# Performance work log

Hardware: AMD Instinct MI355X
Metric: run time of the kernel (lower is better)

The kernel has to match this reference:

```python
import jax, jax.numpy as jnp
import numpy as np

D_MODEL = 1024
H = 16
D_K = D_MODEL // H
D_FF = 4096
EPS = 1e-6
NEG = -1.0e9


def setup_inputs() -> dict:
    key = jax.random.key(0)
    ks = jax.random.split(key, 8)
    B, S = 4, 2048
    x = jax.random.normal(ks[0], (B, S, D_MODEL), dtype=jnp.float32)
    src_mask = jnp.ones((B, 1, S, S), dtype=jnp.int32)
    s = 0.02
    wq = jax.random.normal(ks[1], (D_MODEL, D_MODEL), jnp.float32) * s
    wk = jax.random.normal(ks[2], (D_MODEL, D_MODEL), jnp.float32) * s
    wv = jax.random.normal(ks[3], (D_MODEL, D_MODEL), jnp.float32) * s
    wo = jax.random.normal(ks[4], (D_MODEL, D_MODEL), jnp.float32) * s
    w1 = jax.random.normal(ks[5], (D_MODEL, D_FF), jnp.float32) * s
    b1 = jnp.zeros((D_FF,), jnp.float32)
    w2 = jax.random.normal(ks[6], (D_FF, D_MODEL), jnp.float32) * s
    b2 = jnp.zeros((D_MODEL,), jnp.float32)
    # LayerNorm params are scalars in the original (torch.ones(1)/zeros(1))
    a1 = jnp.ones((1,), jnp.float32); bt1 = jnp.zeros((1,), jnp.float32)
    a2 = jnp.ones((1,), jnp.float32); bt2 = jnp.zeros((1,), jnp.float32)
    return {"x": x, "src_mask": src_mask, "wq": wq, "wk": wk, "wv": wv,
            "wo": wo, "w1": w1, "b1": b1, "w2": w2, "b2": b2,
            "a1": a1, "bt1": bt1, "a2": a2, "bt2": bt2}


def _layernorm(x, alpha, beta):
    # Original: (x - mean) / (std + eps), std with Bessel correction (torch default)
    mean = jnp.mean(x, axis=-1, keepdims=True)
    std = jnp.std(x, axis=-1, keepdims=True, ddof=1)
    return alpha * (x - mean) / (std + EPS) + beta


def _mha(x, mask, wq, wk, wv, wo):
    B, S, _ = x.shape
    q = (x @ wq).reshape(B, S, H, D_K).transpose(0, 2, 1, 3)  # [B,H,S,Dk]
    k = (x @ wk).reshape(B, S, H, D_K).transpose(0, 2, 1, 3)
    v = (x @ wv).reshape(B, S, H, D_K).transpose(0, 2, 1, 3)
    scores = jnp.einsum('bhqd,bhkd->bhqk', q, k) / jnp.sqrt(jnp.float32(D_K))
    scores = jnp.where(mask == 0, NEG, scores)
    attn = jax.nn.softmax(scores, axis=-1)
    out = jnp.einsum('bhqk,bhkd->bhqd', attn, v)  # [B,H,S,Dk]
    out = out.transpose(0, 2, 1, 3).reshape(B, S, D_MODEL)
    return out @ wo


def reference(x, src_mask, wq, wk, wv, wo, w1, b1, w2, b2, a1, bt1, a2, bt2):
    # Sublayer 1: self-attention with post-norm residual (dropout = eval/identity)
    attn_out = _mha(x, src_mask, wq, wk, wv, wo)
    x = _layernorm(x + attn_out, a1, bt1)
    # Sublayer 2: FFN with post-norm residual
    ffn_out = jax.nn.relu(x @ w1 + b1) @ w2 + b2
    x = _layernorm(x + ffn_out, a2, bt2)
    return x
```

## Files before the change

kernel.cpp:

```cpp
#include <hip/hip_runtime.h>
#include <stdint.h>

typedef __bf16 bf16x8 __attribute__((ext_vector_type(8)));
typedef float f32x4 __attribute__((ext_vector_type(4)));
typedef float f32x16 __attribute__((ext_vector_type(16)));
typedef unsigned short u16;
typedef u16 u16x8 __attribute__((ext_vector_type(8)));
typedef u16 u16x4 __attribute__((ext_vector_type(4)));
typedef uint32_t u32;

#define DEV __device__ __forceinline__
#define MFMA(a, b, c) __builtin_amdgcn_mfma_f32_16x16x32_bf16(a, b, c, 0, 0, 0)
#define MFMA32(a, b, c) __builtin_amdgcn_mfma_f32_32x32x16_bf16(a, b, c, 0, 0, 0)

static constexpr int B_ = 4, S_ = 2048, M_ = 8192, D_ = 1024, H_ = 16, DFF_ = 4096;

DEV u16 f2bf(float f) {
    union { float f; u32 u; } c; c.f = f;
    u32 u = c.u;
    return (u16)((u + 0x7fffu + ((u >> 16) & 1u)) >> 16);
}

DEV float bf2f(u16 v) {
    union { u32 u; float f; } c; c.u = (u32)v << 16;
    return c.f;
}

DEV u32 cvt_pk_bf16(float lo, float hi) {
    u32 r;
    asm("v_cvt_pk_bf16_f32 %0, %1, %2" : "=v"(r) : "v"(lo), "v"(hi));
    return r;
}

DEV float v_exp2(float x) {
    float r;
    asm("v_exp_f32 %0, %1" : "=v"(r) : "v"(x));
    return r;
}

DEV void gload16(void* lds, const void* g) {
    __builtin_amdgcn_global_load_lds(
        (const __attribute__((address_space(1))) unsigned int*)g,
        (__attribute__((address_space(3))) unsigned int*)lds, 16, 0, 0);
}


__global__ __launch_bounds__(256) void k_pack_amask(const int* __restrict__ m,
                                                    u32* __restrict__ bits,
                                                    u32* __restrict__ am) {
    const int lane = threadIdx.x & 63, wv = threadIdx.x >> 6;
    const int row = blockIdx.x * 4 + wv;
    const int4* s = (const int4*)(m + ((size_t)row * 64 + lane) * 32);
    u32 r = 0;
#pragma unroll
    for (int j = 0; j < 8; j++) {
        int4 v = s[j];
        r |= (u32)(v.x != 0) << (j * 4) | (u32)(v.y != 0) << (j * 4 + 1) |
             (u32)(v.z != 0) << (j * 4 + 2) | (u32)(v.w != 0) << (j * 4 + 3);
    }
    bits[(size_t)row * 64 + lane] = r;
    unsigned long long b = __ballot(r == 0xffffffffu);
    if (lane == 0) {
        u32 a = 0;
#pragma unroll
        for (int t = 0; t < 32; t++)
            a |= (u32)(((b >> (2 * t)) & 3ull) == 3ull) << t;
        am[row] = a;
    }
}

__global__ __launch_bounds__(256) void k_cast_bf16(const float* __restrict__ s,
                                                   u16* __restrict__ d, int n4) {
    int i = blockIdx.x * 256 + threadIdx.x;
    if (i >= n4) return;
    f32x4 v = ((const f32x4*)s)[i];
    u16x4 o;
    o[0] = f2bf(v[0]); o[1] = f2bf(v[1]); o[2] = f2bf(v[2]); o[3] = f2bf(v[3]);
    ((u16x4*)d)[i] = o;
}

__global__ void k_transpose_cast(const float* __restrict__ s, u16* __restrict__ d,
                                 int K, int N) {
    __shared__ float t[32][33];
    int n0 = blockIdx.x * 32, k0 = blockIdx.y * 32;
    int tx = threadIdx.x, ty = threadIdx.y;
#pragma unroll
    for (int i = 0; i < 4; i++)
        t[ty + i * 8][tx] = s[(size_t)(k0 + ty + i * 8) * N + n0 + tx];
    __syncthreads();
#pragma unroll
    for (int i = 0; i < 4; i++)
        d[(size_t)(n0 + ty + i * 8) * K + k0 + tx] = f2bf(t[tx][ty + i * 8]);
}

__global__ void k_transpose_cast4(const float* __restrict__ s0,
                                  const float* __restrict__ s1,
                                  const float* __restrict__ s2,
                                  const float* __restrict__ s3,
                                  u16* __restrict__ dbase) {
    __shared__ float t[32][33];
    const int z = blockIdx.z;
    const float* s = (z == 0) ? s0 : (z == 1) ? s1 : (z == 2) ? s2 : s3;
    u16* d = dbase + (size_t)z * D_ * D_;
    int n0 = blockIdx.x * 32, k0 = blockIdx.y * 32;
    int tx = threadIdx.x, ty = threadIdx.y;
#pragma unroll
    for (int i = 0; i < 4; i++)
        t[ty + i * 8][tx] = s[(size_t)(k0 + ty + i * 8) * D_ + n0 + tx];
    __syncthreads();
#pragma unroll
    for (int i = 0; i < 4; i++)
        d[(size_t)(n0 + ty + i * 8) * D_ + k0 + tx] = f2bf(t[tx][ty + i * 8]);
}

template <int EPI>
__global__ __launch_bounds__(512, 4) void k_gemm8(const u16* __restrict__ A,
                                                  const u16* __restrict__ Bt,
                                                  float* __restrict__ Cf,
                                                  u16* __restrict__ Cb,
                                                  const float* __restrict__ bias,
                                                  const float* __restrict__ resid,
                                                  u16* __restrict__ Vt,
                                                  int N, int K) {
    __shared__ u16 As[2][128 * 64];
    __shared__ u16 Bs[2][128 * 64];
    const int tid = threadIdx.x, lane = tid & 63, wave = tid >> 6;
    const int lr = lane & 15, lg = lane >> 4;
    const int wm = wave >> 1, wn = wave & 1;
    const int nbx = N >> 7;
    const int chunk = gridDim.x >> 3;
    const int id = ((int)blockIdx.x & 7) * chunk + ((int)blockIdx.x >> 3);
    const size_t row0 = (size_t)(id / nbx) * 128;
    const int col0 = (id % nbx) * 128;
    const int srow = lane >> 3;
    const int sgr = (lane & 7) ^ srow;
    const int NT = K >> 6;
    f32x4 acc[2][4] = {};

    auto stage = [&](int buf, int t) {
#pragma unroll
        for (int i = 0; i < 2; i++) {
            int c = i * 8 + wave;
            gload16((char*)&As[buf][0] + c * 1024,
                    (const char*)(A + (row0 + c * 8 + srow) * K + t * 64 + sgr * 8));
        }
#pragma unroll
        for (int i = 0; i < 2; i++) {
            int c = i * 8 + wave;
            gload16((char*)&Bs[buf][0] + c * 1024,
                    (const char*)(Bt + (size_t)(col0 + c * 8 + srow) * K + t * 64 + sgr * 8));
        }
    };

    stage(0, 0);
    for (int t = 0; t < NT; ++t) {
        const int cur = t & 1;
        if (t + 1 < NT) {
            stage(cur ^ 1, t + 1);
            asm volatile("s_waitcnt vmcnt(4)" ::: "memory");
        } else {
            asm volatile("s_waitcnt vmcnt(0)" ::: "memory");
        }
        __builtin_amdgcn_s_barrier();
        asm volatile("" ::: "memory");
        bf16x8 bF[4][2];
#pragma unroll
        for (int n = 0; n < 4; n++) {
            int r = wn * 64 + n * 16 + lr;
            int rb = r * 128, sw = (r & 7) << 4;
#pragma unroll
            for (int ks = 0; ks < 2; ks++)
                bF[n][ks] = *(const bf16x8*)((char*)&Bs[cur][0] +
                                             (rb + ((ks * 64 + lg * 16) ^ sw)));
        }
#pragma unroll
        for (int m = 0; m < 2; m++) {
            int r = wm * 32 + m * 16 + lr;
            int rb = r * 128, sw = (r & 7) << 4;
            bf16x8 a0 = *(const bf16x8*)((char*)&As[cur][0] + (rb + ((lg * 16) ^ sw)));
            bf16x8 a1 = *(const bf16x8*)((char*)&As[cur][0] + (rb + ((64 + lg * 16) ^ sw)));
            __builtin_amdgcn_s_setprio(1);
#pragma unroll
            for (int n = 0; n < 4; n++) {
                acc[m][n] = MFMA(a0, bF[n][0], acc[m][n]);
                acc[m][n] = MFMA(a1, bF[n][1], acc[m][n]);
            }
            __builtin_amdgcn_s_setprio(0);
        }
        asm volatile("" ::: "memory");
        __builtin_amdgcn_s_barrier();
    }
#pragma unroll
    for (int m = 0; m < 2; m++)
#pragma unroll
        for (int n = 0; n < 4; n++) {
            const int cg = col0 + wn * 64 + n * 16 + lr;
            const int rbase = (int)row0 + wm * 32 + m * 16 + lg * 4;
            if constexpr (EPI == 0) {
                const int proj = cg >> 10, hh = (cg >> 6) & 15, dk = cg & 63;
                const int b = rbase >> 11, s = rbase & 2047;
                if (proj == 2) {
                    u16x4 ov;
#pragma unroll
                    for (int i = 0; i < 4; i++) ov[i] = f2bf(acc[m][n][i]);
                    *(u16x4*)(Vt + ((size_t)(b * 16 + hh) * 64 + dk) * 2048 + s) = ov;
                } else {
                    const float sc = (proj == 0) ? 0.1803368801111832f : 1.f;
                    size_t base = ((size_t)(proj * 64 + b * 16 + hh) * 2048 + s) * 64 + dk;
#pragma unroll
                    for (int i = 0; i < 4; i++)
                        Cb[base + (size_t)i * 64] = f2bf(acc[m][n][i] * sc);
                }
            } else {
#pragma unroll
                for (int i = 0; i < 4; i++) {
                    const int rg = rbase + i;
                    float v = acc[m][n][i];
                    if constexpr (EPI == 1) {
                        Cb[(size_t)rg * N + cg] = f2bf(v + resid[(size_t)rg * N + cg]);
                    } else if constexpr (EPI == 2) {
                        v += bias[cg];
                        v = v > 0.f ? v : 0.f;
                        Cb[(size_t)rg * N + cg] = f2bf(v);
                    } else {
                        Cf[(size_t)rg * N + cg] = v + bias[cg] + resid[(size_t)rg * N + cg];
                    }
                }
            }
        }
}

template <int EPI, int KSPLITS>
__global__ __launch_bounds__(512, 2) void k_gemm256(const u16* __restrict__ A,
                                                    const u16* __restrict__ Bt,
                                                    u16* __restrict__ Cb,
                                                    u16* __restrict__ Cb2,
                                                    const float* __restrict__ bias,
                                                    int N, int Keff, int lda) {
    __shared__ u16 As[2][256 * 64];
    __shared__ u16 Bs[2][256 * 64];
    const int tid = threadIdx.x, lane = tid & 63, wave = tid >> 6;
    const int lr = lane & 15, lg = lane >> 4;
    const int wm = wave >> 2, wn = wave & 3;
    const int nbx = N >> 8;
    const int chunk = gridDim.x >> 3;
    const int id = ((int)blockIdx.x & 7) * chunk + ((int)blockIdx.x >> 3);
    int tileid = id, ksplit = 0;
    if constexpr (KSPLITS == 2) { ksplit = id & 1; tileid = id >> 1; }
    const int kof = ksplit * Keff;
    const size_t row0 = (size_t)(tileid / nbx) * 256;
    const int col0 = (tileid % nbx) * 256;
    const int srow = lane >> 3;
    const int sgr = (lane & 7) ^ srow;
    const int NT = Keff >> 6;
    f32x4 acc[8][4] = {};

    auto stage_half = [&](int isB, int buf, int t, int h) {
        const u16* g = isB ? Bt : A;
        const size_t grow0 = isB ? (size_t)col0 : row0;
        char* base = isB ? (char*)&Bs[buf][0] : (char*)&As[buf][0];
#pragma unroll
        for (int l = 0; l < 2; l++) {
            int rt = h * 128 + l * 64 + wave * 8;
            gload16(base + rt * 128,
                    (const char*)(g + (grow0 + rt + srow) * lda + kof + t * 64 + sgr * 8));
        }
    };
    auto rdA = [&](int cur, int mh, int m, int kk) -> bf16x8 {
        int r = wm * 128 + mh * 64 + m * 16 + lr;
        int gi = kk * 4 + lg;
        return *(const bf16x8*)((char*)&As[cur][0] + r * 128 + ((gi ^ (r & 7)) << 4));
    };
    auto rdB = [&](int cur, int nh, int n, int kk) -> bf16x8 {
        int r = wn * 64 + nh * 32 + n * 16 + lr;
        int gi = kk * 4 + lg;
        return *(const bf16x8*)((char*)&Bs[cur][0] + r * 128 + ((gi ^ (r & 7)) << 4));
    };

    stage_half(0, 0, 0, 0); stage_half(0, 0, 0, 1);
    stage_half(1, 0, 0, 0); stage_half(1, 0, 0, 1);
    stage_half(1, 1, 1, 0); stage_half(1, 1, 1, 1);
    asm volatile("s_waitcnt vmcnt(4)" ::: "memory");
    __builtin_amdgcn_s_barrier();

    bf16x8 aF[4][2], b0F[2][2], b1F[2][2];
    for (int t = 0; t < NT; ++t) {
        const int cur = t & 1, nxt = cur ^ 1;
#pragma unroll
        for (int m = 0; m < 4; m++) { aF[m][0] = rdA(cur, 0, m, 0); aF[m][1] = rdA(cur, 0, m, 1); }
#pragma unroll
        for (int n = 0; n < 2; n++) { b0F[n][0] = rdB(cur, 0, n, 0); b0F[n][1] = rdB(cur, 0, n, 1); }
        if (t + 1 < NT) stage_half(0, nxt, t + 1, 0);
        __builtin_amdgcn_s_barrier();
        asm volatile("s_waitcnt lgkmcnt(0)" ::: "memory");
        __builtin_amdgcn_sched_barrier(0);
        __builtin_amdgcn_s_setprio(1);
#pragma unroll
        for (int m = 0; m < 4; m++)
#pragma unroll
            for (int n = 0; n < 2; n++) {
                acc[m][n] = MFMA(aF[m][0], b0F[n][0], acc[m][n]);
                acc[m][n] = MFMA(aF[m][1], b0F[n][1], acc[m][n]);
            }
        __builtin_amdgcn_s_setprio(0);
        __builtin_amdgcn_s_barrier();
#pragma unroll
        for (int n = 0; n < 2; n++) { b1F[n][0] = rdB(cur, 1, n, 0); b1F[n][1] = rdB(cur, 1, n, 1); }
        if (t + 1 < NT) stage_half(0, nxt, t + 1, 1);
        __builtin_amdgcn_s_barrier();
        asm volatile("s_waitcnt lgkmcnt(0)" ::: "memory");
        __builtin_amdgcn_sched_barrier(0);
        __builtin_amdgcn_s_setprio(1);
#pragma unroll
        for (int m = 0; m < 4; m++)
#pragma unroll
            for (int n = 0; n < 2; n++) {
                acc[m][2 + n] = MFMA(aF[m][0], b1F[n][0], acc[m][2 + n]);
                acc[m][2 + n] = MFMA(aF[m][1], b1F[n][1], acc[m][2 + n]);
            }
        __builtin_amdgcn_s_setprio(0);
        __builtin_amdgcn_s_barrier();
#pragma unroll
        for (int m = 0; m < 4; m++) { aF[m][0] = rdA(cur, 1, m, 0); aF[m][1] = rdA(cur, 1, m, 1); }
        if (t + 2 < NT) stage_half(1, cur, t + 2, 0);
        __builtin_amdgcn_s_barrier();
        asm volatile("s_waitcnt lgkmcnt(0)" ::: "memory");
        __builtin_amdgcn_sched_barrier(0);
        __builtin_amdgcn_s_setprio(1);
#pragma unroll
        for (int m = 0; m < 4; m++)
#pragma unroll
            for (int n = 0; n < 2; n++) {
                acc[4 + m][2 + n] = MFMA(aF[m][0], b1F[n][0], acc[4 + m][2 + n]);
                acc[4 + m][2 + n] = MFMA(aF[m][1], b1F[n][1], acc[4 + m][2 + n]);
            }
        __builtin_amdgcn_s_setprio(0);
        __builtin_amdgcn_s_barrier();
        if (t + 2 < NT) stage_half(1, cur, t + 2, 1);
        if (t + 1 < NT) {
            if (t + 2 < NT) asm volatile("s_waitcnt vmcnt(4)" ::: "memory");
            else            asm volatile("s_waitcnt vmcnt(0)" ::: "memory");
        }
        __builtin_amdgcn_s_barrier();
        __builtin_amdgcn_s_setprio(1);
#pragma unroll
        for (int m = 0; m < 4; m++)
#pragma unroll
            for (int n = 0; n < 2; n++) {
                acc[4 + m][n] = MFMA(aF[m][0], b0F[n][0], acc[4 + m][n]);
                acc[4 + m][n] = MFMA(aF[m][1], b0F[n][1], acc[4 + m][n]);
            }
        __builtin_amdgcn_s_setprio(0);
        __builtin_amdgcn_s_barrier();
    }
    u16* Cout = (KSPLITS == 2 && ksplit) ? Cb2 : Cb;
#pragma unroll
    for (int m = 0; m < 8; m++)
#pragma unroll
        for (int n = 0; n < 4; n++)
#pragma unroll
            for (int i = 0; i < 4; i++) {
                int rg = (int)row0 + wm * 128 + m * 16 + lg * 4 + i;
                int cg = col0 + wn * 64 + n * 16 + lr;
                float v = acc[m][n][i];
                if constexpr (EPI == 2) {
                    v += bias[cg];
                    v = v > 0.f ? v : 0.f;
                    Cout[(size_t)rg * N + cg] = f2bf(v);
                } else {
                    Cout[(size_t)rg * N + cg] = f2bf(v);
                }
            }
}

__global__ __launch_bounds__(256) void k_attn(const u16* __restrict__ qkv,
                                              const u16* __restrict__ vT,
                                              const u32* __restrict__ mbits,
                                              const u32* __restrict__ amask,
                                              u16* __restrict__ outb) {
    __shared__ u16 Kt[2][64 * 64];
    __shared__ u16 Vt[2][64 * 64];
    const int tid = threadIdx.x, lane = tid & 63, wave = tid >> 6;
    const int l31 = lane & 31, hi = lane >> 5;
    const int id0 = blockIdx.y * 16 + blockIdx.x;
    const int id = (id0 & 7) * 128 + (id0 >> 3);
    const int bh = id >> 4;
    const int b = bh >> 4, h = bh & 15;
    const int qb0 = (id & 15) * 128;
    const size_t qbase = (size_t)bh * (2048 * 64);
    const size_t kbase = (size_t)(64 + bh) * (2048 * 64);
    const size_t vtbase = (size_t)bh * (64 * 2048);

    bf16x8 qf[4];
    const int q0 = qb0 + wave * 32;
#pragma unroll
    for (int dstep = 0; dstep < 4; dstep++)
        qf[dstep] = *(const bf16x8*)(qkv + qbase + (size_t)(q0 + l31) * 64 +
                                     dstep * 16 + hi * 8);

    u16x8 ones_u;
#pragma unroll
    for (int e = 0; e < 8; e++) ones_u[e] = 0x3f80;
    const bf16x8 ones8 = *(const bf16x8*)&ones_u;

    f32x16 o0 = {}, o1 = {}, lacc = {};
    f32x16 zin;
#pragma unroll
    for (int r = 0; r < 16; r++) zin[r] = -16.f;

    const int str = tid >> 2, sq = tid & 3;
    const int swzs = (str & 7) << 4;

    u16x8 krA, krB, vrA, vrB;
    auto issue_loads = [&](int kv0n) {
        const u16* ksrc = qkv + kbase + (size_t)(kv0n + str) * 64 + sq * 16;
        krA = *(const u16x8*)ksrc; krB = *(const u16x8*)(ksrc + 8);
        const u16* vsrc = vT + vtbase + (size_t)str * 2048 + kv0n + sq * 16;
        vrA = *(const u16x8*)vsrc; vrB = *(const u16x8*)(vsrc + 8);
    };
    auto write_tile = [&](int buf) {
        int b0 = str * 128 + sq * 32;
        *(u16x8*)((char*)&Kt[buf][0] + ((b0) ^ swzs)) = krA;
        *(u16x8*)((char*)&Kt[buf][0] + ((b0 + 16) ^ swzs)) = krB;
        *(u16x8*)((char*)&Vt[buf][0] + ((b0) ^ swzs)) = vrA;
        *(u16x8*)((char*)&Vt[buf][0] + ((b0 + 16) ^ swzs)) = vrB;
    };

    const u32 am = amask[b * 2048 + qb0 + wave * 32 + l31];
    const int rK0 = l31, rK1 = 32 + l31;
    const int swK0 = (rK0 & 7) << 4, swK1 = (rK1 & 7) << 4;

    issue_loads(0);
    write_tile(0);
    for (int t = 0; t < 32; ++t) {
        const int cur = t & 1;
        if (t + 1 < 32) issue_loads((t + 1) * 64);
        asm volatile("s_waitcnt lgkmcnt(0)" ::: "memory");
        __builtin_amdgcn_s_barrier();

        f32x16 st0 = zin, st1 = zin;
        __builtin_amdgcn_s_setprio(1);
#pragma unroll
        for (int dstep = 0; dstep < 4; dstep++) {
            bf16x8 kf0 = *(const bf16x8*)((char*)&Kt[cur][0] + rK0 * 128 +
                                          ((dstep * 32 + hi * 16) ^ swK0));
            bf16x8 kf1 = *(const bf16x8*)((char*)&Kt[cur][0] + rK1 * 128 +
                                          ((dstep * 32 + hi * 16) ^ swK1));
            st0 = MFMA32(kf0, qf[dstep], st0);
            st1 = MFMA32(kf1, qf[dstep], st1);
        }
        __builtin_amdgcn_s_setprio(0);

        if (!((am >> t) & 1u)) {
            uint2 mw = *(const uint2*)&mbits[(size_t)(b * 2048 + qb0 + wave * 32 + l31) * 64 + 2 * t];
            u32 mw0 = mw.x >> (hi * 4), mw1 = mw.y >> (hi * 4);
#pragma unroll
            for (int r = 0; r < 16; r++) {
                int sh = (r & 3) + 8 * (r >> 2);
                if (!((mw0 >> sh) & 1u)) st0[r] = -1e9f;
                if (!((mw1 >> sh) & 1u)) st1[r] = -1e9f;
            }
        }
        bf16x8 pa[4];
#pragma unroll
        for (int r = 0; r < 16; r++) { st0[r] = v_exp2(st0[r]); st1[r] = v_exp2(st1[r]); }
#pragma unroll
        for (int kvb = 0; kvb < 2; kvb++) {
            const f32x16& st = kvb ? st1 : st0;
            u32 wA[4], wB[4];
#pragma unroll
            for (int g = 0; g < 4; g++) {
                wA[g] = cvt_pk_bf16(st[4 * g], st[4 * g + 1]);
                wB[g] = cvt_pk_bf16(st[4 * g + 2], st[4 * g + 3]);
            }
#pragma unroll
            for (int s = 0; s < 2; s++) {
                u32 xA = wA[2 * s], yA = wA[2 * s + 1];
                asm("v_permlane32_swap_b32 %0, %1" : "+v"(xA), "+v"(yA));
                u32 xB = wB[2 * s], yB = wB[2 * s + 1];
                asm("v_permlane32_swap_b32 %0, %1" : "+v"(xB), "+v"(yB));
                union { u32 w[4]; bf16x8 v; } pk;
                pk.w[0] = xA; pk.w[1] = xB; pk.w[2] = yA; pk.w[3] = yB;
                pa[kvb * 2 + s] = pk.v;
            }
        }
        __builtin_amdgcn_s_setprio(1);
#pragma unroll
        for (int ks = 0; ks < 4; ks++) {
            bf16x8 vb0 = *(const bf16x8*)((char*)&Vt[cur][0] + rK0 * 128 +
                                          ((ks * 32 + hi * 16) ^ swK0));
            bf16x8 vb1 = *(const bf16x8*)((char*)&Vt[cur][0] + rK1 * 128 +
                                          ((ks * 32 + hi * 16) ^ swK1));
            lacc = MFMA32(pa[ks], ones8, lacc);
            o0 = MFMA32(pa[ks], vb0, o0);
            o1 = MFMA32(pa[ks], vb1, o1);
        }
        __builtin_amdgcn_s_setprio(0);
        if (t + 1 < 32) write_tile(cur ^ 1);
    }
#pragma unroll
    for (int r = 0; r < 16; r++) {
        float inv = 1.f / lacc[r];
        int qg = qb0 + wave * 32 + (r & 3) + 8 * (r >> 2) + 4 * hi;
        size_t rowb = (size_t)(b * 2048 + qg) * 1024 + h * 64 + l31;
        outb[rowb] = f2bf(o0[r] * inv);
        outb[rowb + 32] = f2bf(o1[r] * inv);
    }
}

__global__ __launch_bounds__(256) void k_ln_b(const u16* __restrict__ tin,
                                              u16* __restrict__ outb,
                                              const float* __restrict__ alpha,
                                              const float* __restrict__ beta) {
    const int row = blockIdx.x, tid = threadIdx.x;
    const u16x4 tv = ((const u16x4*)(tin + (size_t)row * 1024))[tid];
    f32x4 t;
#pragma unroll
    for (int i = 0; i < 4; i++) t[i] = bf2f(tv[i]);
    float s = t[0] + t[1] + t[2] + t[3];
    float ss = t[0] * t[0] + t[1] * t[1] + t[2] * t[2] + t[3] * t[3];
#pragma unroll
    for (int m2 = 1; m2 < 64; m2 <<= 1) {
        s += __shfl_xor(s, m2);
        ss += __shfl_xor(ss, m2);
    }
    __shared__ float ps[4], pss[4];
    if ((tid & 63) == 0) { ps[tid >> 6] = s; pss[tid >> 6] = ss; }
    __syncthreads();
    s = ps[0] + ps[1] + ps[2] + ps[3];
    ss = pss[0] + pss[1] + pss[2] + pss[3];
    const float mean = s * (1.f / 1024.f);
    float var = (ss - 1024.f * mean * mean) * (1.f / 1023.f);
    var = fmaxf(var, 0.f);
    const float inv = alpha[0] / (sqrtf(var) + 1e-6f);
    const float bet = beta[0];
    u16x4 ob;
#pragma unroll
    for (int i = 0; i < 4; i++) ob[i] = f2bf((t[i] - mean) * inv + bet);
    ((u16x4*)(outb + (size_t)row * 1024))[tid] = ob;
}

__global__ __launch_bounds__(256) void k_ln_sum2(const u16* __restrict__ p0,
                                                 const u16* __restrict__ p1,
                                                 const u16* __restrict__ residb,
                                                 const float* __restrict__ bias,
                                                 float* __restrict__ outf,
                                                 const float* __restrict__ alpha,
                                                 const float* __restrict__ beta) {
    const int row = blockIdx.x, tid = threadIdx.x;
    const u16x4 av = ((const u16x4*)(p0 + (size_t)row * 1024))[tid];
    const u16x4 cv = ((const u16x4*)(p1 + (size_t)row * 1024))[tid];
    const u16x4 rv = ((const u16x4*)(residb + (size_t)row * 1024))[tid];
    const f32x4 bb = ((const f32x4*)bias)[tid];
    f32x4 t;
#pragma unroll
    for (int i = 0; i < 4; i++) t[i] = bf2f(av[i]) + bf2f(cv[i]) + bf2f(rv[i]) + bb[i];
    float s = t[0] + t[1] + t[2] + t[3];
    float ss = t[0] * t[0] + t[1] * t[1] + t[2] * t[2] + t[3] * t[3];
#pragma unroll
    for (int m2 = 1; m2 < 64; m2 <<= 1) {
        s += __shfl_xor(s, m2);
        ss += __shfl_xor(ss, m2);
    }
    __shared__ float ps[4], pss[4];
    if ((tid & 63) == 0) { ps[tid >> 6] = s; pss[tid >> 6] = ss; }
    __syncthreads();
    s = ps[0] + ps[1] + ps[2] + ps[3];
    ss = pss[0] + pss[1] + pss[2] + pss[3];
    const float mean = s * (1.f / 1024.f);
    float var = (ss - 1024.f * mean * mean) * (1.f / 1023.f);
    var = fmaxf(var, 0.f);
    const float inv = alpha[0] / (sqrtf(var) + 1e-6f);
    const float bet = beta[0];
    f32x4 oo;
#pragma unroll
    for (int i = 0; i < 4; i++) oo[i] = (t[i] - mean) * inv + bet;
    ((f32x4*)(outf + (size_t)row * 1024))[tid] = oo;
}

extern "C" void kernel_launch(void* const* d_in, const int* in_sizes, int n_in,
                              void* d_out, int out_size, void* d_ws, size_t ws_size,
                              hipStream_t stream) {
    const float* x   = (const float*)d_in[0];
    const int*   msk = (const int*)d_in[1];
    const float* wq  = (const float*)d_in[2];
    const float* wk  = (const float*)d_in[3];
    const float* wv  = (const float*)d_in[4];
    const float* wo  = (const float*)d_in[5];
    const float* w1  = (const float*)d_in[6];
    const float* b1  = (const float*)d_in[7];
    const float* w2  = (const float*)d_in[8];
    const float* b2  = (const float*)d_in[9];
    const float* a1  = (const float*)d_in[10];
    const float* bt1 = (const float*)d_in[11];
    const float* a2  = (const float*)d_in[12];
    const float* bt2 = (const float*)d_in[13];
    float* out = (float*)d_out;

    char* ws = (char*)d_ws;
    size_t off = 0;
    auto alloc = [&](size_t bytes) {
        void* p = ws + off;
        off += (bytes + 255) & ~(size_t)255;
        return p;
    };
    u16* xb    = (u16*)alloc((size_t)M_ * D_ * 2);
    u16* wqkvT = (u16*)alloc((size_t)3 * D_ * D_ * 2);
    u16* woT   = (u16*)alloc((size_t)D_ * D_ * 2);
    u16* w1T   = (u16*)alloc((size_t)DFF_ * D_ * 2);
    u16* w2T   = (u16*)alloc((size_t)D_ * DFF_ * 2);
    u32* mbits = (u32*)alloc((size_t)B_ * S_ * 64 * 4);
    u32* amsk  = (u32*)alloc((size_t)B_ * S_ * 4);
    u16* aout  = (u16*)alloc((size_t)M_ * D_ * 2);
    u16* yb    = (u16*)alloc((size_t)M_ * D_ * 2);
    u16* y0b   = (u16*)alloc((size_t)M_ * D_ * 2);
    u16* y1b   = (u16*)alloc((size_t)M_ * D_ * 2);
    u16* x1b   = (u16*)alloc((size_t)M_ * D_ * 2);
    u16* vTb   = (u16*)alloc((size_t)64 * 64 * 2048 * 2);
    u16* qkv   = (u16*)alloc((size_t)M_ * DFF_ * 2);
    u16* hft   = qkv;

    k_pack_amask<<<dim3((B_ * S_) / 4), 256, 0, stream>>>(msk, mbits, amsk);
    k_cast_bf16<<<dim3((M_ * D_ / 4) / 256), 256, 0, stream>>>(x, xb, M_ * D_ / 4);
    dim3 tb(32, 8);
    k_transpose_cast4<<<dim3(32, 32, 4), tb, 0, stream>>>(wq, wk, wv, wo, wqkvT);
    k_transpose_cast<<<dim3(128, 32), tb, 0, stream>>>(w1, w1T, D_, DFF_);
    k_transpose_cast<<<dim3(32, 128), tb, 0, stream>>>(w2, w2T, DFF_, D_);

    k_gemm8<0><<<dim3(1536), 512, 0, stream>>>(xb, wqkvT, nullptr, qkv, nullptr,
                                               nullptr, vTb, 3 * D_, D_);
    k_attn<<<dim3(16, 64), 256, 0, stream>>>(qkv, vTb, mbits, amsk, aout);
    k_gemm8<1><<<dim3(512), 512, 0, stream>>>(aout, woT, nullptr, yb, nullptr, x,
                                              nullptr, D_, D_);
    k_ln_b<<<dim3(M_), 256, 0, stream>>>(yb, x1b, a1, bt1);
    k_gemm256<2, 1><<<dim3(512), 512, 0, stream>>>(x1b, w1T, hft, nullptr,
                                                   b1, DFF_, D_, D_);
    k_gemm256<3, 2><<<dim3(256), 512, 0, stream>>>(hft, w2T, y0b, y1b,
                                                   nullptr, D_, DFF_ / 2, DFF_);
    k_ln_sum2<<<dim3(M_), 256, 0, stream>>>(y0b, y1b, x1b, b2, out, a2, bt2);
}
```

Measured before the change: 392.8 us.

## Use 512-thread attention blocks covering 256 queries; read bf16 residual in Wo GEMM

Each attention block now has 8 waves covering 256 query rows instead of 4 waves covering 128. Every K/V tile staged into shared memory is therefore reused by twice as many queries, and each thread loads one 16-byte vector per tile instead of two. Separately, the output-projection epilogue adds the residual from the bf16 copy of x rather than the fp32 input, which halves the residual read traffic at a small precision cost. The change also removes the unused fp32 epilogue path from the GEMM. The larger attention blocks raise per-block register pressure and leave fewer blocks in the grid.

```diff
diff --git a/kernel.cpp b/kernel.cpp
--- a/kernel.cpp
+++ b/kernel.cpp
@@ -116,10 +116,9 @@
 template <int EPI>
 __global__ __launch_bounds__(512, 4) void k_gemm8(const u16* __restrict__ A,
                                                   const u16* __restrict__ Bt,
-                                                  float* __restrict__ Cf,
                                                   u16* __restrict__ Cb,
                                                   const float* __restrict__ bias,
-                                                  const float* __restrict__ resid,
+                                                  const u16* __restrict__ residb,
                                                   u16* __restrict__ Vt,
                                                   int N, int K) {
     __shared__ u16 As[2][128 * 64];
@@ -217,13 +216,12 @@
                     const int rg = rbase + i;
                     float v = acc[m][n][i];
                     if constexpr (EPI == 1) {
-                        Cb[(size_t)rg * N + cg] = f2bf(v + resid[(size_t)rg * N + cg]);
-                    } else if constexpr (EPI == 2) {
+                        Cb[(size_t)rg * N + cg] =
+                            f2bf(v + bf2f(residb[(size_t)rg * N + cg]));
+                    } else {
                         v += bias[cg];
                         v = v > 0.f ? v : 0.f;
                         Cb[(size_t)rg * N + cg] = f2bf(v);
-                    } else {
-                        Cf[(size_t)rg * N + cg] = v + bias[cg] + resid[(size_t)rg * N + cg];
                     }
                 }
             }
@@ -373,7 +371,7 @@
             }
 }
 
-__global__ __launch_bounds__(256) void k_attn(const u16* __restrict__ qkv,
+__global__ __launch_bounds__(512) void k_attn(const u16* __restrict__ qkv,
                                               const u16* __restrict__ vT,
                                               const u32* __restrict__ mbits,
                                               const u32* __restrict__ amask,
@@ -382,11 +380,11 @@
     __shared__ u16 Vt[2][64 * 64];
     const int tid = threadIdx.x, lane = tid & 63, wave = tid >> 6;
     const int l31 = lane & 31, hi = lane >> 5;
-    const int id0 = blockIdx.y * 16 + blockIdx.x;
-    const int id = (id0 & 7) * 128 + (id0 >> 3);
-    const int bh = id >> 4;
+    const int id0 = blockIdx.y * 8 + blockIdx.x;
+    const int id = (id0 & 7) * 64 + (id0 >> 3);
+    const int bh = id >> 3;
     const int b = bh >> 4, h = bh & 15;
-    const int qb0 = (id & 15) * 128;
+    const int qb0 = (id & 7) * 256;
     const size_t qbase = (size_t)bh * (2048 * 64);
     const size_t kbase = (size_t)(64 + bh) * (2048 * 64);
     const size_t vtbase = (size_t)bh * (64 * 2048);
@@ -408,22 +406,18 @@
 #pragma unroll
     for (int r = 0; r < 16; r++) zin[r] = -16.f;
 
-    const int str = tid >> 2, sq = tid & 3;
-    const int swzs = (str & 7) << 4;
-
-    u16x8 krA, krB, vrA, vrB;
+    const int srow = tid >> 3, sg8 = tid & 7;
+    const int swzs = (srow & 7) << 4;
+    const int sb0 = srow * 128 + sg8 * 16;
+
+    u16x8 krA, vrA;
     auto issue_loads = [&](int kv0n) {
-        const u16* ksrc = qkv + kbase + (size_t)(kv0n + str) * 64 + sq * 16;
-        krA = *(const u16x8*)ksrc; krB = *(const u16x8*)(ksrc + 8);
-        const u16* vsrc = vT + vtbase + (size_t)str * 2048 + kv0n + sq * 16;
-        vrA = *(const u16x8*)vsrc; vrB = *(const u16x8*)(vsrc + 8);
+        krA = *(const u16x8*)(qkv + kbase + (size_t)(kv0n + srow) * 64 + sg8 * 8);
+        vrA = *(const u16x8*)(vT + vtbase + (size_t)srow * 2048 + kv0n + sg8 * 8);
     };
     auto write_tile = [&](int buf) {
-        int b0 = str * 128 + sq * 32;
-        *(u16x8*)((char*)&Kt[buf][0] + ((b0) ^ swzs)) = krA;
-        *(u16x8*)((char*)&Kt[buf][0] + ((b0 + 16) ^ swzs)) = krB;
-        *(u16x8*)((char*)&Vt[buf][0] + ((b0) ^ swzs)) = vrA;
-        *(u16x8*)((char*)&Vt[buf][0] + ((b0 + 16) ^ swzs)) = vrB;
+        *(u16x8*)((char*)&Kt[buf][0] + (sb0 ^ swzs)) = krA;
+        *(u16x8*)((char*)&Vt[buf][0] + (sb0 ^ swzs)) = vrA;
     };
 
     const u32 am = amask[b * 2048 + qb0 + wave * 32 + l31];
@@ -627,10 +621,10 @@
     k_transpose_cast<<<dim3(128, 32), tb, 0, stream>>>(w1, w1T, D_, DFF_);
     k_transpose_cast<<<dim3(32, 128), tb, 0, stream>>>(w2, w2T, DFF_, D_);
 
-    k_gemm8<0><<<dim3(1536), 512, 0, stream>>>(xb, wqkvT, nullptr, qkv, nullptr,
+    k_gemm8<0><<<dim3(1536), 512, 0, stream>>>(xb, wqkvT, qkv, nullptr,
                                                nullptr, vTb, 3 * D_, D_);
-    k_attn<<<dim3(16, 64), 256, 0, stream>>>(qkv, vTb, mbits, amsk, aout);
-    k_gemm8<1><<<dim3(512), 512, 0, stream>>>(aout, woT, nullptr, yb, nullptr, x,
+    k_attn<<<dim3(8, 64), 512, 0, stream>>>(qkv, vTb, mbits, amsk, aout);
+    k_gemm8<1><<<dim3(512), 512, 0, stream>>>(aout, woT, yb, nullptr, xb,
                                               nullptr, D_, D_);
     k_ln_b<<<dim3(M_), 256, 0, stream>>>(yb, x1b, a1, bt1);
     k_gemm256<2, 1><<<dim3(512), 512, 0, stream>>>(x1b, w1T, hft, nullptr,
```

Result: faster. 372.0 us, median of 2 (-5.3%).
